# Optimization experiments

Measured on AMD Instinct MI355X. Metric: run time of the kernel, lower is better.

Reference implementation:

```python
import jax, jax.numpy as jnp
import numpy as np

GLYPH_DIM = 4096
PADDING_IDX = GLYPH_DIM  # 4096
GLYPH_EMB = 20           # CHAR_EMB 16 + COLOR_EMB 4
HIDDEN = 32
MAX_LEN = 64


def setup_inputs() -> dict:
    key = jax.random.key(0)
    k1, k2, k3, k4, k5, k6, k7 = jax.random.split(key, 7)
    B, H, W = 8192, 21, 79
    glyph_chars = jax.random.randint(k1, (B, H, W), 0, 256, dtype=jnp.int32)
    glyph_colors = jax.random.randint(k2, (B, H, W), 0, 16, dtype=jnp.int32)
    # Embedding table with zero padding row (torch padding_idx semantics)
    emb_table = jax.random.normal(k3, (GLYPH_DIM + 1, GLYPH_EMB), dtype=jnp.float32) * 0.02
    emb_table = emb_table.at[PADDING_IDX].set(0.0)
    s = 1.0 / np.sqrt(HIDDEN)
    W_ih = jax.random.uniform(k4, (HIDDEN, GLYPH_EMB), minval=-s, maxval=s, dtype=jnp.float32)
    W_hh = jax.random.uniform(k5, (HIDDEN, HIDDEN), minval=-s, maxval=s, dtype=jnp.float32)
    b_ih = jax.random.uniform(k6, (HIDDEN,), minval=-s, maxval=s, dtype=jnp.float32)
    b_hh = jax.random.uniform(k7, (HIDDEN,), minval=-s, maxval=s, dtype=jnp.float32)
    return {"glyph_chars": glyph_chars, "glyph_colors": glyph_colors,
            "emb_table": emb_table, "W_ih": W_ih, "W_hh": W_hh,
            "b_ih": b_ih, "b_hh": b_hh}


def _encode_bag(glyph_chars, glyph_colors):
    """Batched sorted-unique compaction over the bounded glyph id range."""
    B = glyph_chars.shape[0]
    g_ids = ((glyph_chars << 4) + glyph_colors).reshape(B, -1)  # [B, H*W]
    # presence[b, g] = glyph g appears in sample b (batched histogram)
    bidx = jnp.broadcast_to(jnp.arange(B, dtype=g_ids.dtype)[:, None], g_ids.shape)
    presence = jnp.zeros((B, GLYPH_DIM), dtype=bool).at[bidx, g_ids].set(True)
    # compact: present ids keep their value, absent become PADDING_IDX (=4096),
    # so sorting yields ascending unique ids followed by padding.
    ids = jnp.arange(GLYPH_DIM, dtype=jnp.int32)
    keys = jnp.where(presence, ids, jnp.int32(PADDING_IDX))
    bag = jnp.sort(keys, axis=1)[:, :MAX_LEN]  # [B, MAX_LEN]
    lengths = jnp.minimum(presence.sum(axis=1), MAX_LEN)  # [B]
    return bag, lengths


def reference(glyph_chars, glyph_colors, emb_table, W_ih, W_hh, b_ih, b_hh):
    bag, lengths = _encode_bag(glyph_chars, glyph_colors)
    emb = emb_table[bag]  # [B, MAX_LEN, GLYPH_EMB]
    B = emb.shape[0]

    # packed RNN == plain RNN where hidden state freezes past each sequence length
    xs = jnp.swapaxes(emb, 0, 1)  # [T, B, E]

    def step(h, inp):
        xt, t = inp
        h_new = jnp.tanh(xt @ W_ih.T + b_ih + h @ W_hh.T + b_hh)
        h = jnp.where((t < lengths)[:, None], h_new, h)
        return h, None

    h0 = jnp.zeros((B, HIDDEN), dtype=emb.dtype)
    h, _ = jax.lax.scan(step, h0, (xs, jnp.arange(MAX_LEN)))
    return (h, emb, bag)
```

## Files before the change

### kernel.cpp

```cpp
#include <hip/hip_runtime.h>

#define HW 1659
#define PADID 4096
#define EMB 20
#define HID 32
#define MAXLEN 64
#define PROJ_BLOCKS 128

typedef float v2f __attribute__((ext_vector_type(2)));

template <int CTRL>
__device__ __forceinline__ float dppf(float v) {
    return __builtin_bit_cast(float,
        __builtin_amdgcn_update_dpp(0, __builtin_bit_cast(int, v),
                                    CTRL, 0xF, 0xF, true));
}
#define DPP_XOR1 0xB1
#define DPP_XOR2 0x4E
#define DPP_XOR7 0x141
#define DPP_XORF 0x140

__global__ __launch_bounds__(128, 4) void bag_emb_kernel(
    const int* __restrict__ chars, const int* __restrict__ colors,
    const float* __restrict__ emb_table, const float* __restrict__ W_ih,
    float* __restrict__ out_emb, float* __restrict__ out_bag,
    float* __restrict__ proj, int nbag)
{
    const int tid = threadIdx.x;

    if ((int)blockIdx.x >= nbag) {
        const int gid = ((int)blockIdx.x - nbag) * 128 + tid;
        const int NP = (PADID + 1) * HID;
        for (int idx = gid; idx < NP; idx += PROJ_BLOCKS * 128) {
            const int g = idx >> 5, j = idx & 31;
            const float* er = emb_table + (size_t)g * EMB;
            const float* wr = W_ih + j * EMB;
            float s = 0.f;
#pragma unroll
            for (int k = 0; k < EMB; k++) s += wr[k] * er[k];
            proj[idx] = s;
        }
        return;
    }

    __shared__ __align__(16) unsigned char pres[4096];
    __shared__ int bagl[64];
    __shared__ int wsum[2];

    const int lane = tid & 63;
    const int wv   = tid >> 6;
    const int b    = blockIdx.x;

    const int base = b * HW;
    const int pe = (4 - (base & 3)) & 3;
    const int nv = (HW - pe) >> 2;
    const int nt = HW - pe - (nv << 2);
    const int4* c4 = (const int4*)(chars + base + pe);
    const int4* k4 = (const int4*)(colors + base + pe);

    int4 ca0 = c4[tid],       ka0 = k4[tid];
    int4 ca1 = c4[tid + 128], ka1 = k4[tid + 128];
    int4 ca2 = c4[tid + 256], ka2 = k4[tid + 256];
    const bool has3 = (tid + 384) < nv;
    const int i3 = has3 ? tid + 384 : tid;
    int4 ca3 = c4[i3], ka3 = k4[i3];
    int gp = -1, gt = -1;
    if (tid < pe) gp = (chars[base + tid] << 4) + colors[base + tid];
    if (tid < nt) {
        const int i = base + pe + (nv << 2) + tid;
        gt = (chars[i] << 4) + colors[i];
    }

    ((uint4*)pres)[tid]       = make_uint4(0u, 0u, 0u, 0u);
    ((uint4*)pres)[tid + 128] = make_uint4(0u, 0u, 0u, 0u);
    if (tid < 64) bagl[tid] = PADID;
    __syncthreads();

    pres[(ca0.x << 4) + ka0.x] = 1;
    pres[(ca0.y << 4) + ka0.y] = 1;
    pres[(ca0.z << 4) + ka0.z] = 1;
    pres[(ca0.w << 4) + ka0.w] = 1;
    pres[(ca1.x << 4) + ka1.x] = 1;
    pres[(ca1.y << 4) + ka1.y] = 1;
    pres[(ca1.z << 4) + ka1.z] = 1;
    pres[(ca1.w << 4) + ka1.w] = 1;
    pres[(ca2.x << 4) + ka2.x] = 1;
    pres[(ca2.y << 4) + ka2.y] = 1;
    pres[(ca2.z << 4) + ka2.z] = 1;
    pres[(ca2.w << 4) + ka2.w] = 1;
    if (has3) {
        pres[(ca3.x << 4) + ka3.x] = 1;
        pres[(ca3.y << 4) + ka3.y] = 1;
        pres[(ca3.z << 4) + ka3.z] = 1;
        pres[(ca3.w << 4) + ka3.w] = 1;
    }
    if (gp >= 0) pres[gp] = 1;
    if (gt >= 0) pres[gt] = 1;
    __syncthreads();

    const unsigned M = 0x01010101u;
    int base_cnt = 0;
#pragma unroll 1
    for (int r = 0; r < 2; r++) {
        const uint4 w = ((const uint4*)pres)[tid + (r << 7)];
        const int cnt = __popc(w.x & M) + __popc(w.y & M)
                      + __popc(w.z & M) + __popc(w.w & M);
        int pre = cnt;
#pragma unroll
        for (int d = 1; d < 64; d <<= 1) {
            const int v = __shfl_up(pre, d, 64);
            if (lane >= d) pre += v;
        }
        if (lane == 63) wsum[wv] = pre;
        __syncthreads();
        const int w0 = wsum[0], w1 = wsum[1];
        int p = base_cnt + (wv ? w0 : 0) + pre - cnt;
        if (p < 64) {
            const unsigned wrd[4] = {w.x, w.y, w.z, w.w};
            const int idbase = (r << 11) + (tid << 4);
#pragma unroll
            for (int c = 0; c < 4; c++) {
#pragma unroll
                for (int k = 0; k < 4; k++) {
                    if ((wrd[c] >> (8 * k)) & 1) {
                        if (p < 64) bagl[p] = idbase + 4 * c + k;
                        p++;
                    }
                }
            }
        }
        base_cnt += w0 + w1;
        if (base_cnt >= 64) break;
        __syncthreads();
    }
    __syncthreads();

    if (tid < 64) out_bag[(size_t)b * 64 + tid] = (float)bagl[tid];

    const float4* tab4 = (const float4*)emb_table;
    float4* dst4 = (float4*)(out_emb + (size_t)b * (MAXLEN * EMB));
#pragma unroll
    for (int m = 0; m < 3; m++) {
        const int q = tid + (m << 7);
        if (q < MAXLEN * 5) {
            const int t = q / 5;
            const int mm = q - t * 5;
            const int row = bagl[t];
            dst4[q] = tab4[row * 5 + mm];
        }
    }
}

__global__ __launch_bounds__(128)
__attribute__((amdgpu_waves_per_eu(2, 2)))
void rnn_kernel(
    const float* __restrict__ proj, const float* __restrict__ bagf,
    const float* __restrict__ W_hh,
    const float* __restrict__ b_ih, const float* __restrict__ b_hh,
    float* __restrict__ out_h)
{
    const int tid  = threadIdx.x;
    const int wv   = tid >> 6;
    const int lane = tid & 63;
    const int sl   = lane >> 4;
    const int ib   = wv * 4 + sl;
    const int jj   = lane & 15;
    const int b    = blockIdx.x * 8 + ib;

    const int GMAP[16] = {0,1,2,3, 7,6,5,4, 15,14,13,12,11,10,9,8};

    v2f w0[16], w1[16];
    const float2* wr0 = (const float2*)(W_hh + (2 * jj) * HID);
    const float2* wr1 = (const float2*)(W_hh + (2 * jj + 1) * HID);
#pragma unroll
    for (int m = 0; m < 16; m++) {
        const int c = jj ^ GMAP[m];
        float2 a = wr0[c], bb = wr1[c];
        w0[m] = (v2f){a.x, a.y};
        w1[m] = (v2f){bb.x, bb.y};
    }
    const float sb0 = b_ih[2 * jj]     + b_hh[2 * jj];
    const float sb1 = b_ih[2 * jj + 1] + b_hh[2 * jj + 1];

    const float* bps = bagf + (size_t)b * 64;
    const float2* proj2 = (const float2*)proj;

    float h0 = 0.f, h1 = 0.f;

#pragma unroll
    for (int ch = 0; ch < 4; ch++) {
        int idx[16];
#pragma unroll
        for (int i = 0; i < 16; i++) idx[i] = (int)bps[ch * 16 + i];
        float2 pv[16];
#pragma unroll
        for (int i = 0; i < 16; i++) pv[i] = proj2[idx[i] * 16 + jj];

#pragma unroll
        for (int i = 0; i < 16; i++) {
            const bool upd = idx[i] < PADID;

            v2f g[16];
            g[0] = (v2f){h0, h1};
            g[1] = (v2f){dppf<DPP_XOR1>(g[0].x), dppf<DPP_XOR1>(g[0].y)};
            g[2] = (v2f){dppf<DPP_XOR2>(g[0].x), dppf<DPP_XOR2>(g[0].y)};
            g[3] = (v2f){dppf<DPP_XOR2>(g[1].x), dppf<DPP_XOR2>(g[1].y)};
#pragma unroll
            for (int m = 0; m < 4; m++)
                g[4 + m] = (v2f){dppf<DPP_XOR7>(g[m].x), dppf<DPP_XOR7>(g[m].y)};
#pragma unroll
            for (int m = 0; m < 8; m++)
                g[8 + m] = (v2f){dppf<DPP_XORF>(g[m].x), dppf<DPP_XORF>(g[m].y)};

            v2f a0 = (v2f){0.f, 0.f}, b0 = a0, a1 = a0, b1 = a0;
#pragma unroll
            for (int m = 0; m < 16; m += 2) {
                a0 = __builtin_elementwise_fma(w0[m],     g[m],     a0);
                b0 = __builtin_elementwise_fma(w0[m + 1], g[m + 1], b0);
                a1 = __builtin_elementwise_fma(w1[m],     g[m],     a1);
                b1 = __builtin_elementwise_fma(w1[m + 1], g[m + 1], b1);
            }
            float s0 = sb0 + pv[i].x + (a0.x + a0.y) + (b0.x + b0.y);
            float s1 = sb1 + pv[i].y + (a1.x + a1.y) + (b1.x + b1.y);

            float e0 = __expf(2.f * s0);
            float e1 = __expf(2.f * s1);
            float th0 = 1.f - 2.f * __builtin_amdgcn_rcpf(e0 + 1.f);
            float th1 = 1.f - 2.f * __builtin_amdgcn_rcpf(e1 + 1.f);

            h0 = upd ? th0 : h0;
            h1 = upd ? th1 : h1;
        }
    }

    ((float2*)(out_h + (size_t)b * HID))[jj] = make_float2(h0, h1);
}

__global__ __launch_bounds__(128, 4) void rnn_kernel_noproj(
    const float* __restrict__ emb, const float* __restrict__ bagf,
    const float* __restrict__ W_ih, const float* __restrict__ W_hh,
    const float* __restrict__ b_ih, const float* __restrict__ b_hh,
    float* __restrict__ out_h)
{
    __shared__ float hbuf[4][32];
    const int tid = threadIdx.x;
    const int ib  = tid >> 5;
    const int j   = tid & 31;
    const int b   = blockIdx.x * 4 + ib;

    float wih[EMB];
#pragma unroll
    for (int k = 0; k < EMB; k++) wih[k] = W_ih[j * EMB + k];
    float whh[HID];
#pragma unroll
    for (int k = 0; k < HID; k++) whh[k] = W_hh[j * HID + k];
    const float sbias = b_ih[j] + b_hh[j];

    const float* bp = bagf + (size_t)b * 64;
    unsigned long long m0 = __ballot(bp[j]      < 4095.5f);
    unsigned long long m1 = __ballot(bp[32 + j] < 4095.5f);
    const int half = ib & 1;
    const int len = __popc((unsigned)(m0 >> (half * 32)))
                  + __popc((unsigned)(m1 >> (half * 32)));

    hbuf[ib][j] = 0.f;
    asm volatile("s_waitcnt lgkmcnt(0)" ::: "memory");

    float h = 0.f;
    const float* xb = emb + (size_t)b * (MAXLEN * EMB);
    for (int t = 0; t < MAXLEN; t++) {
        const float4* xp = (const float4*)(xb + t * EMB);
        float4 x0 = xp[0], x1 = xp[1], x2 = xp[2], x3 = xp[3], x4 = xp[4];
        float s = sbias;
        const float4* hb4 = (const float4*)hbuf[ib];
#pragma unroll
        for (int m = 0; m < 8; m++) {
            float4 hv = hb4[m];
            s += whh[4*m+0]*hv.x + whh[4*m+1]*hv.y
               + whh[4*m+2]*hv.z + whh[4*m+3]*hv.w;
        }
        s += wih[0]*x0.x + wih[1]*x0.y + wih[2]*x0.z + wih[3]*x0.w;
        s += wih[4]*x1.x + wih[5]*x1.y + wih[6]*x1.z + wih[7]*x1.w;
        s += wih[8]*x2.x + wih[9]*x2.y + wih[10]*x2.z + wih[11]*x2.w;
        s += wih[12]*x3.x + wih[13]*x3.y + wih[14]*x3.z + wih[15]*x3.w;
        s += wih[16]*x4.x + wih[17]*x4.y + wih[18]*x4.z + wih[19]*x4.w;
        s = fminf(fmaxf(s, -9.f), 9.f);
        float e = __expf(2.f * s);
        float th = (e - 1.f) * __builtin_amdgcn_rcpf(e + 1.f);
        h = (t < len) ? th : h;
        hbuf[ib][j] = h;
        asm volatile("s_waitcnt lgkmcnt(0)" ::: "memory");
    }
    out_h[(size_t)b * HID + j] = h;
}

extern "C" void kernel_launch(void* const* d_in, const int* in_sizes, int n_in,
                              void* d_out, int out_size, void* d_ws, size_t ws_size,
                              hipStream_t stream) {
    const int*   chars     = (const int*)d_in[0];
    const int*   colors    = (const int*)d_in[1];
    const float* emb_table = (const float*)d_in[2];
    const float* W_ih      = (const float*)d_in[3];
    const float* W_hh      = (const float*)d_in[4];
    const float* b_ih      = (const float*)d_in[5];
    const float* b_hh      = (const float*)d_in[6];

    const int B = in_sizes[0] / HW;

    float* out     = (float*)d_out;
    float* out_h   = out;
    float* out_emb = out + (size_t)B * HID;
    float* out_bag = out_emb + (size_t)B * MAXLEN * EMB;

    const size_t proj_bytes = (size_t)(PADID + 1) * HID * sizeof(float);

    if (ws_size >= proj_bytes && (B % 8) == 0) {
        float* proj = (float*)d_ws;
        bag_emb_kernel<<<B + PROJ_BLOCKS, 128, 0, stream>>>(
            chars, colors, emb_table, W_ih, out_emb, out_bag, proj, B);
        rnn_kernel<<<B / 8, 128, 0, stream>>>(proj, out_bag, W_hh, b_ih, b_hh, out_h);
    } else {
        bag_emb_kernel<<<B, 128, 0, stream>>>(
            chars, colors, emb_table, W_ih, out_emb, out_bag, (float*)d_ws, B);
        rnn_kernel_noproj<<<B / 4, 128, 0, stream>>>(out_emb, out_bag, W_ih, W_hh,
                                                     b_ih, b_hh, out_h);
    }
}
```

Before: 180.2 us.

## Process four samples per block with double-buffered register prefetch of glyph inputs

The bag/embedding kernel now handles four samples per block instead of one. It loads the next sample's chars and colors into registers while the current sample is being compacted in LDS, so global-load latency overlaps with the histogram and scan work. Barriers become explicit lgkmcnt waits plus s_barrier, and launch bounds drop to 3 blocks per CU. In exchange the kernel uses more registers, launches fewer blocks, and hardcodes the per-sample tail lengths, which assumes HW=1659.

```diff
diff --git a/kernel.cpp b/kernel.cpp
--- a/kernel.cpp
+++ b/kernel.cpp
@@ -6,6 +6,7 @@
 #define HID 32
 #define MAXLEN 64
 #define PROJ_BLOCKS 128
+#define SPB 4
 
 typedef float v2f __attribute__((ext_vector_type(2)));
 
@@ -20,11 +21,132 @@
 #define DPP_XOR7 0x141
 #define DPP_XORF 0x140
 
-__global__ __launch_bounds__(128, 4) void bag_emb_kernel(
+__device__ __forceinline__ void bar_lds() {
+    asm volatile("s_waitcnt lgkmcnt(0)" ::: "memory");
+    __builtin_amdgcn_s_barrier();
+}
+
+struct Samp {
+    int4 c0, c1, c2, c3, k0, k1, k2, k3;
+    int gp, gt;
+};
+
+__device__ __forceinline__ void prefetch(Samp& S,
+    const int* __restrict__ chars, const int* __restrict__ colors,
+    int b, int tid)
+{
+    const int base = b * HW;
+    const int pe = (4 - (base & 3)) & 3;
+    const int nt = 3 - pe;
+    const int4* c4 = (const int4*)(chars + base + pe);
+    const int4* k4 = (const int4*)(colors + base + pe);
+
+    S.c0 = c4[tid];       S.k0 = k4[tid];
+    S.c1 = c4[tid + 128]; S.k1 = k4[tid + 128];
+    S.c2 = c4[tid + 256]; S.k2 = k4[tid + 256];
+    const int i3 = (tid < 30) ? tid + 384 : tid;
+    S.c3 = c4[i3];        S.k3 = k4[i3];
+
+    S.gp = -1; S.gt = -1;
+    if (tid < pe) S.gp = (chars[base + tid] << 4) + colors[base + tid];
+    if (tid < nt) {
+        const int i = base + pe + 1656 + tid;
+        S.gt = (chars[i] << 4) + colors[i];
+    }
+    __builtin_amdgcn_sched_barrier(0);
+}
+
+__device__ __forceinline__ void process(const Samp& S,
+    unsigned char* pres, int* bagl, int* wsum,
+    int b, int tid, int lane, int wv,
+    const float* __restrict__ emb_table,
+    float* __restrict__ out_emb, float* __restrict__ out_bag)
+{
+    bar_lds();
+
+    ((uint4*)pres)[tid]       = make_uint4(0u, 0u, 0u, 0u);
+    ((uint4*)pres)[tid + 128] = make_uint4(0u, 0u, 0u, 0u);
+    if (tid < 64) bagl[tid] = PADID;
+    bar_lds();
+
+    pres[(S.c0.x << 4) + S.k0.x] = 1;
+    pres[(S.c0.y << 4) + S.k0.y] = 1;
+    pres[(S.c0.z << 4) + S.k0.z] = 1;
+    pres[(S.c0.w << 4) + S.k0.w] = 1;
+    pres[(S.c1.x << 4) + S.k1.x] = 1;
+    pres[(S.c1.y << 4) + S.k1.y] = 1;
+    pres[(S.c1.z << 4) + S.k1.z] = 1;
+    pres[(S.c1.w << 4) + S.k1.w] = 1;
+    pres[(S.c2.x << 4) + S.k2.x] = 1;
+    pres[(S.c2.y << 4) + S.k2.y] = 1;
+    pres[(S.c2.z << 4) + S.k2.z] = 1;
+    pres[(S.c2.w << 4) + S.k2.w] = 1;
+    pres[(S.c3.x << 4) + S.k3.x] = 1;
+    pres[(S.c3.y << 4) + S.k3.y] = 1;
+    pres[(S.c3.z << 4) + S.k3.z] = 1;
+    pres[(S.c3.w << 4) + S.k3.w] = 1;
+    if (S.gp >= 0) pres[S.gp] = 1;
+    if (S.gt >= 0) pres[S.gt] = 1;
+    bar_lds();
+
+    const unsigned M = 0x01010101u;
+    int base_cnt = 0;
+#pragma unroll 1
+    for (int r = 0; r < 2; r++) {
+        const uint4 w = ((const uint4*)pres)[tid + (r << 7)];
+        const int cnt = __popc(w.x & M) + __popc(w.y & M)
+                      + __popc(w.z & M) + __popc(w.w & M);
+        int pre = cnt;
+#pragma unroll
+        for (int d = 1; d < 64; d <<= 1) {
+            const int v = __shfl_up(pre, d, 64);
+            if (lane >= d) pre += v;
+        }
+        if (lane == 63) wsum[wv] = pre;
+        bar_lds();
+        const int w0 = wsum[0], w1 = wsum[1];
+        int p = base_cnt + (wv ? w0 : 0) + pre - cnt;
+        if (p < 64) {
+            const unsigned wrd[4] = {w.x, w.y, w.z, w.w};
+            const int idbase = (r << 11) + (tid << 4);
+#pragma unroll
+            for (int c = 0; c < 4; c++) {
+#pragma unroll
+                for (int k = 0; k < 4; k++) {
+                    if ((wrd[c] >> (8 * k)) & 1) {
+                        if (p < 64) bagl[p] = idbase + 4 * c + k;
+                        p++;
+                    }
+                }
+            }
+        }
+        base_cnt += w0 + w1;
+        if (base_cnt >= 64) break;
+        bar_lds();
+    }
+    bar_lds();
+
+    if (tid < 64) out_bag[(size_t)b * 64 + tid] = (float)bagl[tid];
+
+    const float4* tab4 = (const float4*)emb_table;
+    float4* dst4 = (float4*)(out_emb + (size_t)b * (MAXLEN * EMB));
+#pragma unroll
+    for (int m = 0; m < 3; m++) {
+        const int q = tid + (m << 7);
+        if (q < MAXLEN * 5) {
+            const int t = q / 5;
+            const int mm = q - t * 5;
+            const int row = bagl[t];
+            dst4[q] = tab4[row * 5 + mm];
+        }
+    }
+}
+
+__global__ __launch_bounds__(128, 3) void bag_emb_kernel(
     const int* __restrict__ chars, const int* __restrict__ colors,
     const float* __restrict__ emb_table, const float* __restrict__ W_ih,
     float* __restrict__ out_emb, float* __restrict__ out_bag,
-    float* __restrict__ proj, int nbag)
+    float* __restrict__ proj, int nbag, int Btot)
 {
     const int tid = threadIdx.x;
 
@@ -49,106 +171,22 @@
 
     const int lane = tid & 63;
     const int wv   = tid >> 6;
-    const int b    = blockIdx.x;
-
-    const int base = b * HW;
-    const int pe = (4 - (base & 3)) & 3;
-    const int nv = (HW - pe) >> 2;
-    const int nt = HW - pe - (nv << 2);
-    const int4* c4 = (const int4*)(chars + base + pe);
-    const int4* k4 = (const int4*)(colors + base + pe);
-
-    int4 ca0 = c4[tid],       ka0 = k4[tid];
-    int4 ca1 = c4[tid + 128], ka1 = k4[tid + 128];
-    int4 ca2 = c4[tid + 256], ka2 = k4[tid + 256];
-    const bool has3 = (tid + 384) < nv;
-    const int i3 = has3 ? tid + 384 : tid;
-    int4 ca3 = c4[i3], ka3 = k4[i3];
-    int gp = -1, gt = -1;
-    if (tid < pe) gp = (chars[base + tid] << 4) + colors[base + tid];
-    if (tid < nt) {
-        const int i = base + pe + (nv << 2) + tid;
-        gt = (chars[i] << 4) + colors[i];
-    }
-
-    ((uint4*)pres)[tid]       = make_uint4(0u, 0u, 0u, 0u);
-    ((uint4*)pres)[tid + 128] = make_uint4(0u, 0u, 0u, 0u);
-    if (tid < 64) bagl[tid] = PADID;
-    __syncthreads();
-
-    pres[(ca0.x << 4) + ka0.x] = 1;
-    pres[(ca0.y << 4) + ka0.y] = 1;
-    pres[(ca0.z << 4) + ka0.z] = 1;
-    pres[(ca0.w << 4) + ka0.w] = 1;
-    pres[(ca1.x << 4) + ka1.x] = 1;
-    pres[(ca1.y << 4) + ka1.y] = 1;
-    pres[(ca1.z << 4) + ka1.z] = 1;
-    pres[(ca1.w << 4) + ka1.w] = 1;
-    pres[(ca2.x << 4) + ka2.x] = 1;
-    pres[(ca2.y << 4) + ka2.y] = 1;
-    pres[(ca2.z << 4) + ka2.z] = 1;
-    pres[(ca2.w << 4) + ka2.w] = 1;
-    if (has3) {
-        pres[(ca3.x << 4) + ka3.x] = 1;
-        pres[(ca3.y << 4) + ka3.y] = 1;
-        pres[(ca3.z << 4) + ka3.z] = 1;
-        pres[(ca3.w << 4) + ka3.w] = 1;
-    }
-    if (gp >= 0) pres[gp] = 1;
-    if (gt >= 0) pres[gt] = 1;
-    __syncthreads();
-
-    const unsigned M = 0x01010101u;
-    int base_cnt = 0;
-#pragma unroll 1
-    for (int r = 0; r < 2; r++) {
-        const uint4 w = ((const uint4*)pres)[tid + (r << 7)];
-        const int cnt = __popc(w.x & M) + __popc(w.y & M)
-                      + __popc(w.z & M) + __popc(w.w & M);
-        int pre = cnt;
-#pragma unroll
-        for (int d = 1; d < 64; d <<= 1) {
-            const int v = __shfl_up(pre, d, 64);
-            if (lane >= d) pre += v;
-        }
-        if (lane == 63) wsum[wv] = pre;
-        __syncthreads();
-        const int w0 = wsum[0], w1 = wsum[1];
-        int p = base_cnt + (wv ? w0 : 0) + pre - cnt;
-        if (p < 64) {
-            const unsigned wrd[4] = {w.x, w.y, w.z, w.w};
-            const int idbase = (r << 11) + (tid << 4);
-#pragma unroll
-            for (int c = 0; c < 4; c++) {
-#pragma unroll
-                for (int k = 0; k < 4; k++) {
-                    if ((wrd[c] >> (8 * k)) & 1) {
-                        if (p < 64) bagl[p] = idbase + 4 * c + k;
-                        p++;
-                    }
-                }
-            }
-        }
-        base_cnt += w0 + w1;
-        if (base_cnt >= 64) break;
-        __syncthreads();
-    }
-    __syncthreads();
-
-    if (tid < 64) out_bag[(size_t)b * 64 + tid] = (float)bagl[tid];
-
-    const float4* tab4 = (const float4*)emb_table;
-    float4* dst4 = (float4*)(out_emb + (size_t)b * (MAXLEN * EMB));
-#pragma unroll
-    for (int m = 0; m < 3; m++) {
-        const int q = tid + (m << 7);
-        if (q < MAXLEN * 5) {
-            const int t = q / 5;
-            const int mm = q - t * 5;
-            const int row = bagl[t];
-            dst4[q] = tab4[row * 5 + mm];
-        }
-    }
+    const int sb   = (int)blockIdx.x * SPB;
+    const int s0 = min(sb + 0, Btot - 1);
+    const int s1 = min(sb + 1, Btot - 1);
+    const int s2 = min(sb + 2, Btot - 1);
+    const int s3 = min(sb + 3, Btot - 1);
+
+    Samp A, B;
+    prefetch(A, chars, colors, s0, tid);
+    prefetch(B, chars, colors, s1, tid);
+
+    process(A, pres, bagl, wsum, s0, tid, lane, wv, emb_table, out_emb, out_bag);
+    prefetch(A, chars, colors, s2, tid);
+    process(B, pres, bagl, wsum, s1, tid, lane, wv, emb_table, out_emb, out_bag);
+    prefetch(B, chars, colors, s3, tid);
+    process(A, pres, bagl, wsum, s2, tid, lane, wv, emb_table, out_emb, out_bag);
+    process(B, pres, bagl, wsum, s3, tid, lane, wv, emb_table, out_emb, out_bag);
 }
 
 __global__ __launch_bounds__(128)
@@ -306,6 +344,7 @@
     const float* b_hh      = (const float*)d_in[6];
 
     const int B = in_sizes[0] / HW;
+    const int NBAG = (B + SPB - 1) / SPB;
 
     float* out     = (float*)d_out;
     float* out_h   = out;
@@ -316,12 +355,12 @@
 
     if (ws_size >= proj_bytes && (B % 8) == 0) {
         float* proj = (float*)d_ws;
-        bag_emb_kernel<<<B + PROJ_BLOCKS, 128, 0, stream>>>(
-            chars, colors, emb_table, W_ih, out_emb, out_bag, proj, B);
+        bag_emb_kernel<<<NBAG + PROJ_BLOCKS, 128, 0, stream>>>(
+            chars, colors, emb_table, W_ih, out_emb, out_bag, proj, NBAG, B);
         rnn_kernel<<<B / 8, 128, 0, stream>>>(proj, out_bag, W_hh, b_ih, b_hh, out_h);
     } else {
-        bag_emb_kernel<<<B, 128, 0, stream>>>(
-            chars, colors, emb_table, W_ih, out_emb, out_bag, (float*)d_ws, B);
+        bag_emb_kernel<<<NBAG, 128, 0, stream>>>(
+            chars, colors, emb_table, W_ih, out_emb, out_bag, (float*)d_ws, NBAG, B);
         rnn_kernel_noproj<<<B / 4, 128, 0, stream>>>(out_emb, out_bag, W_ih, W_hh,
                                                      b_ih, b_hh, out_h);
     }
```

Measured after the change: 186.0 us. +3.2%, slower.

## Software-pipeline projection gathers in RNN kernel with double-buffered chunks

Applied to the files above, without the earlier changes.

The RNN kernel now loads all 64 bag indices up front as vector loads. It then gathers the per-step input projections in 8-step chunks into two alternating register buffers, with sched_barriers so that the next chunk's gather is issued before the current chunk's recurrence runs. This is meant to hide global-memory gather latency behind the serial tanh recurrence instead of stalling at each 16-step chunk boundary. Launch bounds change from waves_per_eu(2,2) to (128,2). The extra live registers and the fixed schedule may lower occupancy or constrain the compiler.

```diff
diff --git a/kernel.cpp b/kernel.cpp
--- a/kernel.cpp
+++ b/kernel.cpp
@@ -8,6 +8,7 @@
 #define PROJ_BLOCKS 128
 
 typedef float v2f __attribute__((ext_vector_type(2)));
+typedef float v4f __attribute__((ext_vector_type(4)));
 
 template <int CTRL>
 __device__ __forceinline__ float dppf(float v) {
@@ -151,8 +152,61 @@
     }
 }
 
-__global__ __launch_bounds__(128)
-__attribute__((amdgpu_waves_per_eu(2, 2)))
+
+__device__ __forceinline__ void pv_fetch8(
+    const float (&idxf)[64], int c0,
+    const v2f* __restrict__ proj2, int jj, v2f (&pv)[8])
+{
+#pragma unroll
+    for (int i = 0; i < 8; i++) {
+        const int row = (int)idxf[c0 + i];
+        pv[i] = proj2[row * 16 + jj];
+    }
+}
+
+__device__ __forceinline__ void rnn_chunk8(
+    const float (&idxf)[64], int c0, const v2f (&pv)[8],
+    const v2f (&w0)[16], const v2f (&w1)[16],
+    float sb0, float sb1, float& h0, float& h1)
+{
+#pragma unroll
+    for (int i = 0; i < 8; i++) {
+        const bool upd = idxf[c0 + i] < 4095.5f;
+
+        v2f g[16];
+        g[0] = (v2f){h0, h1};
+        g[1] = (v2f){dppf<DPP_XOR1>(g[0][0]), dppf<DPP_XOR1>(g[0][1])};
+        g[2] = (v2f){dppf<DPP_XOR2>(g[0][0]), dppf<DPP_XOR2>(g[0][1])};
+        g[3] = (v2f){dppf<DPP_XOR2>(g[1][0]), dppf<DPP_XOR2>(g[1][1])};
+#pragma unroll
+        for (int m = 0; m < 4; m++)
+            g[4 + m] = (v2f){dppf<DPP_XOR7>(g[m][0]), dppf<DPP_XOR7>(g[m][1])};
+#pragma unroll
+        for (int m = 0; m < 8; m++)
+            g[8 + m] = (v2f){dppf<DPP_XORF>(g[m][0]), dppf<DPP_XORF>(g[m][1])};
+
+        v2f a0 = (v2f){0.f, 0.f}, b0 = a0, a1 = a0, b1 = a0;
+#pragma unroll
+        for (int m = 0; m < 16; m += 2) {
+            a0 = __builtin_elementwise_fma(w0[m],     g[m],     a0);
+            b0 = __builtin_elementwise_fma(w0[m + 1], g[m + 1], b0);
+            a1 = __builtin_elementwise_fma(w1[m],     g[m],     a1);
+            b1 = __builtin_elementwise_fma(w1[m + 1], g[m + 1], b1);
+        }
+        float s0 = sb0 + pv[i][0] + (a0[0] + a0[1]) + (b0[0] + b0[1]);
+        float s1 = sb1 + pv[i][1] + (a1[0] + a1[1]) + (b1[0] + b1[1]);
+
+        float e0 = __expf(2.f * s0);
+        float e1 = __expf(2.f * s1);
+        float th0 = 1.f - 2.f * __builtin_amdgcn_rcpf(e0 + 1.f);
+        float th1 = 1.f - 2.f * __builtin_amdgcn_rcpf(e1 + 1.f);
+
+        h0 = upd ? th0 : h0;
+        h1 = upd ? th1 : h1;
+    }
+}
+
+__global__ __launch_bounds__(128, 2)
 void rnn_kernel(
     const float* __restrict__ proj, const float* __restrict__ bagf,
     const float* __restrict__ W_hh,
@@ -170,68 +224,66 @@
     const int GMAP[16] = {0,1,2,3, 7,6,5,4, 15,14,13,12,11,10,9,8};
 
     v2f w0[16], w1[16];
-    const float2* wr0 = (const float2*)(W_hh + (2 * jj) * HID);
-    const float2* wr1 = (const float2*)(W_hh + (2 * jj + 1) * HID);
+    const v2f* wr0 = (const v2f*)(W_hh + (2 * jj) * HID);
+    const v2f* wr1 = (const v2f*)(W_hh + (2 * jj + 1) * HID);
 #pragma unroll
     for (int m = 0; m < 16; m++) {
         const int c = jj ^ GMAP[m];
-        float2 a = wr0[c], bb = wr1[c];
-        w0[m] = (v2f){a.x, a.y};
-        w1[m] = (v2f){bb.x, bb.y};
-    }
+        w0[m] = wr0[c];
+        w1[m] = wr1[c];
+    }
+#pragma unroll
+    for (int m = 0; m < 16; m++) {
+        asm volatile("" : "+v"(w0[m]));
+        asm volatile("" : "+v"(w1[m]));
+    }
+
     const float sb0 = b_ih[2 * jj]     + b_hh[2 * jj];
     const float sb1 = b_ih[2 * jj + 1] + b_hh[2 * jj + 1];
 
-    const float* bps = bagf + (size_t)b * 64;
-    const float2* proj2 = (const float2*)proj;
+    const v2f* proj2 = (const v2f*)proj;
+
+    v4f q[16];
+    const v4f* bp4 = (const v4f*)(bagf + (size_t)b * 64);
+#pragma unroll
+    for (int t = 0; t < 16; t++) q[t] = bp4[t];
+#pragma unroll
+    for (int t = 0; t < 16; t++) asm volatile("" : "+v"(q[t]));
+    float idxf[64];
+#pragma unroll
+    for (int t = 0; t < 16; t++) {
+        idxf[4 * t + 0] = q[t][0];
+        idxf[4 * t + 1] = q[t][1];
+        idxf[4 * t + 2] = q[t][2];
+        idxf[4 * t + 3] = q[t][3];
+    }
 
     float h0 = 0.f, h1 = 0.f;
-
-#pragma unroll
-    for (int ch = 0; ch < 4; ch++) {
-        int idx[16];
-#pragma unroll
-        for (int i = 0; i < 16; i++) idx[i] = (int)bps[ch * 16 + i];
-        float2 pv[16];
-#pragma unroll
-        for (int i = 0; i < 16; i++) pv[i] = proj2[idx[i] * 16 + jj];
-
-#pragma unroll
-        for (int i = 0; i < 16; i++) {
-            const bool upd = idx[i] < PADID;
-
-            v2f g[16];
-            g[0] = (v2f){h0, h1};
-            g[1] = (v2f){dppf<DPP_XOR1>(g[0].x), dppf<DPP_XOR1>(g[0].y)};
-            g[2] = (v2f){dppf<DPP_XOR2>(g[0].x), dppf<DPP_XOR2>(g[0].y)};
-            g[3] = (v2f){dppf<DPP_XOR2>(g[1].x), dppf<DPP_XOR2>(g[1].y)};
-#pragma unroll
-            for (int m = 0; m < 4; m++)
-                g[4 + m] = (v2f){dppf<DPP_XOR7>(g[m].x), dppf<DPP_XOR7>(g[m].y)};
-#pragma unroll
-            for (int m = 0; m < 8; m++)
-                g[8 + m] = (v2f){dppf<DPP_XORF>(g[m].x), dppf<DPP_XORF>(g[m].y)};
-
-            v2f a0 = (v2f){0.f, 0.f}, b0 = a0, a1 = a0, b1 = a0;
-#pragma unroll
-            for (int m = 0; m < 16; m += 2) {
-                a0 = __builtin_elementwise_fma(w0[m],     g[m],     a0);
-                b0 = __builtin_elementwise_fma(w0[m + 1], g[m + 1], b0);
-                a1 = __builtin_elementwise_fma(w1[m],     g[m],     a1);
-                b1 = __builtin_elementwise_fma(w1[m + 1], g[m + 1], b1);
-            }
-            float s0 = sb0 + pv[i].x + (a0.x + a0.y) + (b0.x + b0.y);
-            float s1 = sb1 + pv[i].y + (a1.x + a1.y) + (b1.x + b1.y);
-
-            float e0 = __expf(2.f * s0);
-            float e1 = __expf(2.f * s1);
-            float th0 = 1.f - 2.f * __builtin_amdgcn_rcpf(e0 + 1.f);
-            float th1 = 1.f - 2.f * __builtin_amdgcn_rcpf(e1 + 1.f);
-
-            h0 = upd ? th0 : h0;
-            h1 = upd ? th1 : h1;
-        }
-    }
+    v2f pvA[8], pvB[8];
+
+    pv_fetch8(idxf, 0,  proj2, jj, pvA);
+    pv_fetch8(idxf, 8,  proj2, jj, pvB);
+    __builtin_amdgcn_sched_barrier(0);
+    rnn_chunk8(idxf, 0,  pvA, w0, w1, sb0, sb1, h0, h1);
+    pv_fetch8(idxf, 16, proj2, jj, pvA);
+    __builtin_amdgcn_sched_barrier(0);
+    rnn_chunk8(idxf, 8,  pvB, w0, w1, sb0, sb1, h0, h1);
+    pv_fetch8(idxf, 24, proj2, jj, pvB);
+    __builtin_amdgcn_sched_barrier(0);
+    rnn_chunk8(idxf, 16, pvA, w0, w1, sb0, sb1, h0, h1);
+    pv_fetch8(idxf, 32, proj2, jj, pvA);
+    __builtin_amdgcn_sched_barrier(0);
+    rnn_chunk8(idxf, 24, pvB, w0, w1, sb0, sb1, h0, h1);
+    pv_fetch8(idxf, 40, proj2, jj, pvB);
+    __builtin_amdgcn_sched_barrier(0);
+    rnn_chunk8(idxf, 32, pvA, w0, w1, sb0, sb1, h0, h1);
+    pv_fetch8(idxf, 48, proj2, jj, pvA);
+    __builtin_amdgcn_sched_barrier(0);
+    rnn_chunk8(idxf, 40, pvB, w0, w1, sb0, sb1, h0, h1);
+    pv_fetch8(idxf, 56, proj2, jj, pvB);
+    __builtin_amdgcn_sched_barrier(0);
+    rnn_chunk8(idxf, 48, pvA, w0, w1, sb0, sb1, h0, h1);
+    rnn_chunk8(idxf, 56, pvB, w0, w1, sb0, sb1, h0, h1);
 
     ((float2*)(out_h + (size_t)b * HID))[jj] = make_float2(h0, h1);
 }
```

After: 183.4 us. About the same (+1.8%).

## Software-pipeline RNN bag index and projection gathers with double buffering

Applied to the files above, without the earlier changes.

Splits the recurrent loop over 64 steps into half-chunks of 8 and alternates two register buffers, so the projection gathers for the next half-chunk are issued while the current half-chunk's recurrence runs. Bag indices are loaded as float4 vectors, and the padding test now compares the float index directly. The loop is no longer fully unrolled (unroll 1), and the waves_per_eu attribute is replaced with launch_bounds(128,2). This is meant to hide gather latency behind the serial dependency chain, at the cost of extra registers and a loop that wraps around and does a redundant prefetch on the final iteration.

```diff
diff --git a/kernel.cpp b/kernel.cpp
--- a/kernel.cpp
+++ b/kernel.cpp
@@ -8,6 +8,7 @@
 #define PROJ_BLOCKS 128
 
 typedef float v2f __attribute__((ext_vector_type(2)));
+typedef float v4f __attribute__((ext_vector_type(4)));
 
 template <int CTRL>
 __device__ __forceinline__ float dppf(float v) {
@@ -151,8 +152,47 @@
     }
 }
 
-__global__ __launch_bounds__(128)
-__attribute__((amdgpu_waves_per_eu(2, 2)))
+
+__device__ __forceinline__ void rnn_step(
+    float idxv, v2f pv,
+    const v2f (&w0)[16], const v2f (&w1)[16],
+    float sb0, float sb1, float& h0, float& h1)
+{
+    const bool upd = idxv < 4095.5f;
+
+    v2f g[16];
+    g[0] = (v2f){h0, h1};
+    g[1] = (v2f){dppf<DPP_XOR1>(g[0][0]), dppf<DPP_XOR1>(g[0][1])};
+    g[2] = (v2f){dppf<DPP_XOR2>(g[0][0]), dppf<DPP_XOR2>(g[0][1])};
+    g[3] = (v2f){dppf<DPP_XOR2>(g[1][0]), dppf<DPP_XOR2>(g[1][1])};
+#pragma unroll
+    for (int m = 0; m < 4; m++)
+        g[4 + m] = (v2f){dppf<DPP_XOR7>(g[m][0]), dppf<DPP_XOR7>(g[m][1])};
+#pragma unroll
+    for (int m = 0; m < 8; m++)
+        g[8 + m] = (v2f){dppf<DPP_XORF>(g[m][0]), dppf<DPP_XORF>(g[m][1])};
+
+    v2f a0 = (v2f){0.f, 0.f}, b0 = a0, a1 = a0, b1 = a0;
+#pragma unroll
+    for (int m = 0; m < 16; m += 2) {
+        a0 = __builtin_elementwise_fma(w0[m],     g[m],     a0);
+        b0 = __builtin_elementwise_fma(w0[m + 1], g[m + 1], b0);
+        a1 = __builtin_elementwise_fma(w1[m],     g[m],     a1);
+        b1 = __builtin_elementwise_fma(w1[m + 1], g[m + 1], b1);
+    }
+    float s0 = sb0 + pv[0] + (a0[0] + a0[1]) + (b0[0] + b0[1]);
+    float s1 = sb1 + pv[1] + (a1[0] + a1[1]) + (b1[0] + b1[1]);
+
+    float e0 = __expf(2.f * s0);
+    float e1 = __expf(2.f * s1);
+    float th0 = 1.f - 2.f * __builtin_amdgcn_rcpf(e0 + 1.f);
+    float th1 = 1.f - 2.f * __builtin_amdgcn_rcpf(e1 + 1.f);
+
+    h0 = upd ? th0 : h0;
+    h1 = upd ? th1 : h1;
+}
+
+__global__ __launch_bounds__(128, 2)
 void rnn_kernel(
     const float* __restrict__ proj, const float* __restrict__ bagf,
     const float* __restrict__ W_hh,
@@ -170,66 +210,68 @@
     const int GMAP[16] = {0,1,2,3, 7,6,5,4, 15,14,13,12,11,10,9,8};
 
     v2f w0[16], w1[16];
-    const float2* wr0 = (const float2*)(W_hh + (2 * jj) * HID);
-    const float2* wr1 = (const float2*)(W_hh + (2 * jj + 1) * HID);
+    const v2f* wr0 = (const v2f*)(W_hh + (2 * jj) * HID);
+    const v2f* wr1 = (const v2f*)(W_hh + (2 * jj + 1) * HID);
 #pragma unroll
     for (int m = 0; m < 16; m++) {
         const int c = jj ^ GMAP[m];
-        float2 a = wr0[c], bb = wr1[c];
-        w0[m] = (v2f){a.x, a.y};
-        w1[m] = (v2f){bb.x, bb.y};
+        w0[m] = wr0[c];
+        w1[m] = wr1[c];
     }
     const float sb0 = b_ih[2 * jj]     + b_hh[2 * jj];
     const float sb1 = b_ih[2 * jj + 1] + b_hh[2 * jj + 1];
 
-    const float* bps = bagf + (size_t)b * 64;
-    const float2* proj2 = (const float2*)proj;
+    const v2f* proj2 = (const v2f*)proj;
+    const float* bp = bagf + (size_t)b * 64;
+    const v4f* bp4 = (const v4f*)bp;
 
     float h0 = 0.f, h1 = 0.f;
 
-#pragma unroll
-    for (int ch = 0; ch < 4; ch++) {
-        int idx[16];
-#pragma unroll
-        for (int i = 0; i < 16; i++) idx[i] = (int)bps[ch * 16 + i];
-        float2 pv[16];
-#pragma unroll
-        for (int i = 0; i < 16; i++) pv[i] = proj2[idx[i] * 16 + jj];
-
-#pragma unroll
-        for (int i = 0; i < 16; i++) {
-            const bool upd = idx[i] < PADID;
-
-            v2f g[16];
-            g[0] = (v2f){h0, h1};
-            g[1] = (v2f){dppf<DPP_XOR1>(g[0].x), dppf<DPP_XOR1>(g[0].y)};
-            g[2] = (v2f){dppf<DPP_XOR2>(g[0].x), dppf<DPP_XOR2>(g[0].y)};
-            g[3] = (v2f){dppf<DPP_XOR2>(g[1].x), dppf<DPP_XOR2>(g[1].y)};
-#pragma unroll
-            for (int m = 0; m < 4; m++)
-                g[4 + m] = (v2f){dppf<DPP_XOR7>(g[m].x), dppf<DPP_XOR7>(g[m].y)};
-#pragma unroll
-            for (int m = 0; m < 8; m++)
-                g[8 + m] = (v2f){dppf<DPP_XORF>(g[m].x), dppf<DPP_XORF>(g[m].y)};
-
-            v2f a0 = (v2f){0.f, 0.f}, b0 = a0, a1 = a0, b1 = a0;
-#pragma unroll
-            for (int m = 0; m < 16; m += 2) {
-                a0 = __builtin_elementwise_fma(w0[m],     g[m],     a0);
-                b0 = __builtin_elementwise_fma(w0[m + 1], g[m + 1], b0);
-                a1 = __builtin_elementwise_fma(w1[m],     g[m],     a1);
-                b1 = __builtin_elementwise_fma(w1[m + 1], g[m + 1], b1);
-            }
-            float s0 = sb0 + pv[i].x + (a0.x + a0.y) + (b0.x + b0.y);
-            float s1 = sb1 + pv[i].y + (a1.x + a1.y) + (b1.x + b1.y);
-
-            float e0 = __expf(2.f * s0);
-            float e1 = __expf(2.f * s1);
-            float th0 = 1.f - 2.f * __builtin_amdgcn_rcpf(e0 + 1.f);
-            float th1 = 1.f - 2.f * __builtin_amdgcn_rcpf(e1 + 1.f);
-
-            h0 = upd ? th0 : h0;
-            h1 = upd ? th1 : h1;
+    float idxA[8], idxB[8];
+    v2f pvA[8], pvB[8];
+
+    {
+        v4f q0 = bp4[0], q1 = bp4[1];
+        idxA[0] = q0[0]; idxA[1] = q0[1]; idxA[2] = q0[2]; idxA[3] = q0[3];
+        idxA[4] = q1[0]; idxA[5] = q1[1]; idxA[6] = q1[2]; idxA[7] = q1[3];
+#pragma unroll
+        for (int i = 0; i < 8; i++)
+            pvA[i] = proj2[(int)idxA[i] * 16 + jj];
+        v4f q2 = bp4[2], q3 = bp4[3];
+        idxB[0] = q2[0]; idxB[1] = q2[1]; idxB[2] = q2[2]; idxB[3] = q2[3];
+        idxB[4] = q3[0]; idxB[5] = q3[1]; idxB[6] = q3[2]; idxB[7] = q3[3];
+    }
+
+#pragma unroll 1
+    for (int c = 0; c < 64; c += 16) {
+        const int nc = (c + 16) & 63;
+
+#pragma unroll
+        for (int i = 0; i < 8; i++)
+            pvB[i] = proj2[(int)idxB[i] * 16 + jj];
+
+#pragma unroll
+        for (int i = 0; i < 8; i++)
+            rnn_step(idxA[i], pvA[i], w0, w1, sb0, sb1, h0, h1);
+
+        {
+            const v4f qa0 = bp4[(nc >> 2) + 0], qa1 = bp4[(nc >> 2) + 1];
+            idxA[0] = qa0[0]; idxA[1] = qa0[1]; idxA[2] = qa0[2]; idxA[3] = qa0[3];
+            idxA[4] = qa1[0]; idxA[5] = qa1[1]; idxA[6] = qa1[2]; idxA[7] = qa1[3];
+        }
+
+#pragma unroll
+        for (int i = 0; i < 8; i++)
+            rnn_step(idxB[i], pvB[i], w0, w1, sb0, sb1, h0, h1);
+
+#pragma unroll
+        for (int i = 0; i < 8; i++)
+            pvA[i] = proj2[(int)idxA[i] * 16 + jj];
+
+        {
+            const v4f qb0 = bp4[(nc >> 2) + 2], qb1 = bp4[(nc >> 2) + 3];
+            idxB[0] = qb0[0]; idxB[1] = qb0[1]; idxB[2] = qb0[2]; idxB[3] = qb0[3];
+            idxB[4] = qb1[0]; idxB[5] = qb1[1]; idxB[6] = qb1[2]; idxB[7] = qb1[3];
         }
     }
 
```

Result: slower. 192.0 us (+6.6%).
